# Optimization experiments

Measured on AMD Instinct MI355X. Metric: run time of the kernel, lower is better.

The kernel has to match this reference:

```python
import jax, jax.numpy as jnp
import numpy as np

B, N, Q, H = 32, 1024, 64, 768


def setup_inputs() -> dict:
    key = jax.random.key(0)
    k1, k2, k3, k4 = jax.random.split(key, 4)
    return {
        "nodes_compress": jax.random.normal(k1, (B, N, H), dtype=jnp.float32),
        "query_compress": jax.random.normal(k2, (B, Q, H), dtype=jnp.float32),
        "nodes_hidden": jax.random.normal(k3, (B, N, H), dtype=jnp.float32),
        # nn.Linear(3H, 1, bias=False).weight flattened to (3H,)
        "w": jax.random.normal(k4, (3 * H,), dtype=jnp.float32) * (1.0 / np.sqrt(3 * H)),
    }


def reference(nodes_compress, query_compress, nodes_hidden, w):
    h = nodes_compress.shape[-1]
    w_n, w_q, w_nq = w[:h], w[h:2 * h], w[2 * h:]
    # Decomposed trilinear similarity: identical to Linear([n, q, n*q]) -> scalar
    sim = (
        (nodes_compress @ w_n)[:, :, None]          # (B, N, 1)
        + (query_compress @ w_q)[:, None, :]        # (B, 1, Q)
        + jnp.einsum("bnh,bqh,h->bnq", nodes_compress, query_compress, w_nq)
    )                                                # (B, N, Q)
    # nodes -> query attention
    a = jax.nn.softmax(sim, axis=-1)                 # (B, N, Q)
    nodes2query = jnp.einsum("bnq,bqh->bnh", a, query_compress)
    # query -> nodes attention (max over query, softmax over nodes)
    b = jax.nn.softmax(jnp.max(sim, axis=-1), axis=-1)  # (B, N)
    q2n = jnp.einsum("bn,bnh->bh", b, nodes_compress)[:, None, :]  # (B, 1, H)
    q2n = jnp.broadcast_to(q2n, nodes_compress.shape)               # (B, N, H)
    return jnp.concatenate(
        [nodes_compress, nodes2query, nodes_compress * nodes2query, nodes_compress * q2n],
        axis=-1,
    )  # (B, N, 4H)
```

## Files before the change

kernel.cpp:

```cpp
#include <hip/hip_runtime.h>
#include <hip/hip_bf16.h>

#define BB 32
#define NN 1024
#define QQ 64
#define HH 768

typedef __attribute__((ext_vector_type(8))) short short8;
typedef __attribute__((ext_vector_type(4))) float f32x4;

__device__ __forceinline__ unsigned short f2b(float f) {
  unsigned int u = __float_as_uint(f);
  unsigned int r = u + 0x7fffu + ((u >> 16) & 1u);
  return (unsigned short)(r >> 16);
}

__global__ void k_prep(const float* __restrict__ qc, const float* __restrict__ w,
                       unsigned short* __restrict__ qwB, unsigned short* __restrict__ qcT,
                       float* __restrict__ sq) {
  int bid = blockIdx.x;
  if (bid < 6144) {
    int idx = bid * 256 + threadIdx.x;
    int h = idx % HH;
    qwB[idx] = f2b(qc[idx] * w[2 * HH + h] + w[h]);
    int q2 = idx & 63;
    int h2 = (idx >> 6) % HH;
    int b2 = idx / (HH * QQ);
    qcT[idx] = f2b(qc[(b2 * QQ + q2) * HH + h2]);
  } else {
    int wid = ((bid - 6144) * 256 + threadIdx.x) >> 6;
    int l = threadIdx.x & 63;
    const float* row = qc + (size_t)wid * HH;
    float s = 0.f;
#pragma unroll
    for (int i = 0; i < 12; ++i) s += row[i * 64 + l] * w[HH + i * 64 + l];
#pragma unroll
    for (int m = 1; m < 64; m <<= 1) s += __shfl_xor(s, m);
    if (l == 0) sq[wid] = s;
  }
}

__global__ __launch_bounds__(256) void k_sim(
    const float* __restrict__ nc, const unsigned short* __restrict__ qwB,
    const float* __restrict__ sq, float* __restrict__ partial,
    float* __restrict__ mtse, unsigned short* __restrict__ probs)
{
  __shared__ char smem[32768];
  unsigned short* aLDS = (unsigned short*)smem;
  unsigned short* bLDS = (unsigned short*)(smem + 16384);
  float* rowmF = (float*)(smem + 16384);
  float* wvF   = (float*)(smem + 16384 + 256);

  const int tid = threadIdx.x;
  const int w = tid >> 6, l = tid & 63;
  const int l15 = l & 15, lg = l >> 4;
  const int b = blockIdx.x >> 4, tile = blockIdx.x & 15;
  const int row0 = tile * 64;

  const float* ncB = nc + (size_t)(b * NN + row0) * HH;
  const unsigned short* qwBb = qwB + (size_t)b * QQ * HH;

  f32x4 acc[4] = {};
  for (int kc = 0; kc < 6; ++kc) {
#pragma unroll
    for (int i = 0; i < 4; ++i) {
      int unit = i * 256 + tid;
      int r = unit >> 4, uu = unit & 15;
      const float* src = ncB + r * HH + kc * 128 + uu * 8;
      float4 f0 = *(const float4*)src;
      float4 f1 = *(const float4*)(src + 4);
      short8 v;
      v[0] = (short)f2b(f0.x); v[1] = (short)f2b(f0.y);
      v[2] = (short)f2b(f0.z); v[3] = (short)f2b(f0.w);
      v[4] = (short)f2b(f1.x); v[5] = (short)f2b(f1.y);
      v[6] = (short)f2b(f1.z); v[7] = (short)f2b(f1.w);
      int off = r * 256 + ((uu * 16) ^ ((r & 7) << 4));
      *(short8*)((char*)aLDS + off) = v;
      short8 bv = *(const short8*)(qwBb + r * HH + kc * 128 + uu * 8);
      *(short8*)((char*)bLDS + off) = bv;
    }
    __syncthreads();
#pragma unroll
    for (int ks = 0; ks < 4; ++ks) {
      int kbyte = ks * 64 + lg * 16;
      int arow = w * 16 + l15;
      short8 af = *(short8*)((char*)aLDS + arow * 256 + (kbyte ^ ((l & 7) << 4)));
#pragma unroll
      for (int nt = 0; nt < 4; ++nt) {
        int brow = nt * 16 + l15;
        short8 bf = *(short8*)((char*)bLDS + brow * 256 + (kbyte ^ ((l & 7) << 4)));
        acc[nt] = __builtin_amdgcn_mfma_f32_16x16x32_bf16(af, bf, acc[nt], 0, 0, 0);
      }
      __asm__ volatile("" ::: "memory");
    }
    __syncthreads();
  }

  unsigned short* pT = probs + (size_t)(b * 16 + tile) * (QQ * QQ);
  float sqv[4];
#pragma unroll
  for (int nt = 0; nt < 4; ++nt) sqv[nt] = sq[b * QQ + nt * 16 + l15];
#pragma unroll
  for (int j = 0; j < 4; ++j) {
    float mm = -1e30f;
#pragma unroll
    for (int nt = 0; nt < 4; ++nt) { acc[nt][j] += sqv[nt]; mm = fmaxf(mm, acc[nt][j]); }
    mm = fmaxf(mm, __shfl_xor(mm, 1));
    mm = fmaxf(mm, __shfl_xor(mm, 2));
    mm = fmaxf(mm, __shfl_xor(mm, 4));
    mm = fmaxf(mm, __shfl_xor(mm, 8));
    float ss = 0.f;
#pragma unroll
    for (int nt = 0; nt < 4; ++nt) { float p = __expf(acc[nt][j] - mm); acc[nt][j] = p; ss += p; }
    ss += __shfl_xor(ss, 1); ss += __shfl_xor(ss, 2);
    ss += __shfl_xor(ss, 4); ss += __shfl_xor(ss, 8);
    float inv = 1.0f / ss;
    int r = w * 16 + lg * 4 + j;
#pragma unroll
    for (int nt = 0; nt < 4; ++nt)
      pT[r * 64 + nt * 16 + l15] = f2b(acc[nt][j] * inv);
    if (l15 == 0) rowmF[r] = mm;
  }
  __syncthreads();

  float m_t = -1e30f;
#pragma unroll
  for (int i = 0; i < 16; ++i) {
    f32x4 v = ((f32x4*)rowmF)[i];
    m_t = fmaxf(m_t, fmaxf(fmaxf(v[0], v[1]), fmaxf(v[2], v[3])));
  }
  if (tid < 64) wvF[tid] = __expf(rowmF[tid] - m_t);
  __syncthreads();
  {
    float sv = wvF[l];
#pragma unroll
    for (int m = 1; m < 64; m <<= 1) sv += __shfl_xor(sv, m);
    if (tid == 0) {
      mtse[(b * 16 + tile) * 2] = m_t;
      mtse[(b * 16 + tile) * 2 + 1] = sv;
    }
  }
  {
    float p0 = 0.f, p1 = 0.f, p2 = 0.f;
    for (int n = 0; n < 64; ++n) {
      float wv = wvF[n];
      const float* pr = ncB + n * HH + tid;
      p0 += wv * pr[0]; p1 += wv * pr[256]; p2 += wv * pr[512];
    }
    float* pp = partial + (size_t)(b * 16 + tile) * HH + tid;
    pp[0] = p0; pp[256] = p1; pp[512] = p2;
  }
}

__global__ void k_comb(const float* __restrict__ partial, const float* __restrict__ mtse,
                       float* __restrict__ q2n) {
  int b = blockIdx.x, t = threadIdx.x;
  float mt[16], se[16];
  float M = -1e30f;
#pragma unroll
  for (int i = 0; i < 16; ++i) {
    mt[i] = mtse[(b * 16 + i) * 2];
    se[i] = mtse[(b * 16 + i) * 2 + 1];
    M = fmaxf(M, mt[i]);
  }
  float denom = 0.f;
#pragma unroll
  for (int i = 0; i < 16; ++i) { mt[i] = __expf(mt[i] - M); denom += mt[i] * se[i]; }
  float inv = 1.0f / denom;
  float a0 = 0.f, a1 = 0.f, a2 = 0.f;
#pragma unroll
  for (int i = 0; i < 16; ++i) {
    const float* pp = partial + (size_t)(b * 16 + i) * HH + t;
    float c = mt[i] * inv;
    a0 += c * pp[0]; a1 += c * pp[256]; a2 += c * pp[512];
  }
  q2n[b * HH + t] = a0;
  q2n[b * HH + t + 256] = a1;
  q2n[b * HH + t + 512] = a2;
}

__global__ __launch_bounds__(256) void k_out(
    const float* __restrict__ nc, const unsigned short* __restrict__ qcT,
    const unsigned short* __restrict__ probs, const float* __restrict__ q2n,
    float* __restrict__ out)
{
  __shared__ char smem[16384];

  const int tid = threadIdx.x;
  const int w = tid >> 6, l = tid & 63;
  const int l15 = l & 15, lg = l >> 4;
  const int b = blockIdx.x >> 5;
  const int tile = (blockIdx.x >> 1) & 15;
  const int hh = blockIdx.x & 1;
  const int row0 = tile * 64;

  const unsigned short* pT = probs + (size_t)(b * 16 + tile) * (QQ * QQ);
  short8 a2[2];
  a2[0] = *(const short8*)((const char*)pT + (w * 16 + l15) * 128 + 0 * 64 + lg * 16);
  a2[1] = *(const short8*)((const char*)pT + (w * 16 + l15) * 128 + 1 * 64 + lg * 16);

  const unsigned short* qcTb = qcT + (size_t)b * HH * QQ;
  const int n = w * 16 + l15;
  const float* ncrow = nc + (size_t)(b * NN + row0 + n) * HH;
  float* orow = out + (size_t)(b * NN + row0 + n) * 3072;
  const float* q2nb = q2n + b * HH;

  for (int hc = hh * 3; hc < hh * 3 + 3; ++hc) {
#pragma unroll
    for (int i = 0; i < 4; ++i) {
      int unit = i * 256 + tid;
      int r = unit >> 3, uu = unit & 7;
      short8 v = *(const short8*)(qcTb + (size_t)(hc * 128 + r) * 64 + uu * 8);
      int off = r * 128 + ((uu * 16) ^ ((r & 7) << 4));
      *(short8*)(smem + off) = v;
    }
    __syncthreads();
#pragma unroll
    for (int hg = 0; hg < 8; ++hg) {
      f32x4 c2 = {};
#pragma unroll
      for (int ks2 = 0; ks2 < 2; ++ks2) {
        int hrow = hg * 16 + l15;
        int kbyte = ks2 * 64 + lg * 16;
        short8 hf = *(short8*)(smem + hrow * 128 + (kbyte ^ ((l & 7) << 4)));
        c2 = __builtin_amdgcn_mfma_f32_16x16x32_bf16(hf, a2[ks2], c2, 0, 0, 0);
      }
      int hbase = hc * 128 + hg * 16 + lg * 4;
      f32x4 ncv = *(const f32x4*)(ncrow + hbase);
      f32x4 qv  = *(const f32x4*)(q2nb + hbase);
      __builtin_nontemporal_store(ncv,       (f32x4*)(orow + hbase));
      __builtin_nontemporal_store(c2,        (f32x4*)(orow + HH + hbase));
      __builtin_nontemporal_store(ncv * c2,  (f32x4*)(orow + 2 * HH + hbase));
      __builtin_nontemporal_store(ncv * qv,  (f32x4*)(orow + 2304 + hbase));
    }
    __syncthreads();
  }
}

extern "C" void kernel_launch(void* const* d_in, const int* in_sizes, int n_in,
                              void* d_out, int out_size, void* d_ws, size_t ws_size,
                              hipStream_t stream) {
  (void)in_sizes; (void)n_in; (void)out_size; (void)ws_size;
  const float* nc = (const float*)d_in[0];
  const float* qc = (const float*)d_in[1];
  const float* w  = (const float*)d_in[3];
  float* out = (float*)d_out;
  char* ws = (char*)d_ws;
  unsigned short* qwB = (unsigned short*)(ws);
  unsigned short* qcT = (unsigned short*)(ws + 3145728);
  float* sqv     = (float*)(ws + 6291456);
  float* partial = (float*)(ws + 6299648);
  float* mtse    = (float*)(ws + 7872512);
  float* q2n     = (float*)(ws + 7876608);
  unsigned short* probs = (unsigned short*)(ws + 7975424);

  k_prep<<<6656, 256, 0, stream>>>(qc, w, qwB, qcT, sqv);
  k_sim<<<512, 256, 0, stream>>>(nc, qwB, sqv, partial, mtse, probs);
  k_comb<<<32, 256, 0, stream>>>(partial, mtse, q2n);
  k_out<<<1024, 256, 0, stream>>>(nc, qcT, probs, q2n, out);
}
```

Baseline: 188.8 us.

## Fuse query weighting into sim kernel, split output kernel finer, drop nontemporal stores

```diff
diff --git a/kernel.cpp b/kernel.cpp
--- a/kernel.cpp
+++ b/kernel.cpp
@@ -16,13 +16,10 @@
 }
 
 __global__ void k_prep(const float* __restrict__ qc, const float* __restrict__ w,
-                       unsigned short* __restrict__ qwB, unsigned short* __restrict__ qcT,
-                       float* __restrict__ sq) {
+                       unsigned short* __restrict__ qcT, float* __restrict__ sq) {
   int bid = blockIdx.x;
   if (bid < 6144) {
     int idx = bid * 256 + threadIdx.x;
-    int h = idx % HH;
-    qwB[idx] = f2b(qc[idx] * w[2 * HH + h] + w[h]);
     int q2 = idx & 63;
     int h2 = (idx >> 6) % HH;
     int b2 = idx / (HH * QQ);
@@ -41,9 +38,10 @@
 }
 
 __global__ __launch_bounds__(256) void k_sim(
-    const float* __restrict__ nc, const unsigned short* __restrict__ qwB,
-    const float* __restrict__ sq, float* __restrict__ partial,
-    float* __restrict__ mtse, unsigned short* __restrict__ probs)
+    const float* __restrict__ nc, const float* __restrict__ qc,
+    const float* __restrict__ w, const float* __restrict__ sq,
+    float* __restrict__ partial, float* __restrict__ mtse,
+    unsigned short* __restrict__ probs)
 {
   __shared__ char smem[32768];
   unsigned short* aLDS = (unsigned short*)smem;
@@ -52,13 +50,13 @@
   float* wvF   = (float*)(smem + 16384 + 256);
 
   const int tid = threadIdx.x;
-  const int w = tid >> 6, l = tid & 63;
+  const int wv_ = tid >> 6, l = tid & 63;
   const int l15 = l & 15, lg = l >> 4;
   const int b = blockIdx.x >> 4, tile = blockIdx.x & 15;
   const int row0 = tile * 64;
 
   const float* ncB = nc + (size_t)(b * NN + row0) * HH;
-  const unsigned short* qwBb = qwB + (size_t)b * QQ * HH;
+  const float* qcB = qc + (size_t)b * QQ * HH;
 
   f32x4 acc[4] = {};
   for (int kc = 0; kc < 6; ++kc) {
@@ -66,7 +64,8 @@
     for (int i = 0; i < 4; ++i) {
       int unit = i * 256 + tid;
       int r = unit >> 4, uu = unit & 15;
-      const float* src = ncB + r * HH + kc * 128 + uu * 8;
+      int h = kc * 128 + uu * 8;
+      const float* src = ncB + r * HH + h;
       float4 f0 = *(const float4*)src;
       float4 f1 = *(const float4*)(src + 4);
       short8 v;
@@ -76,14 +75,25 @@
       v[6] = (short)f2b(f1.z); v[7] = (short)f2b(f1.w);
       int off = r * 256 + ((uu * 16) ^ ((r & 7) << 4));
       *(short8*)((char*)aLDS + off) = v;
-      short8 bv = *(const short8*)(qwBb + r * HH + kc * 128 + uu * 8);
+      const float* qsrc = qcB + r * HH + h;
+      float4 g0 = *(const float4*)qsrc;
+      float4 g1 = *(const float4*)(qsrc + 4);
+      float4 wn0 = *(const float4*)(w + h);
+      float4 wn1 = *(const float4*)(w + h + 4);
+      float4 wm0 = *(const float4*)(w + 2 * HH + h);
+      float4 wm1 = *(const float4*)(w + 2 * HH + h + 4);
+      short8 bv;
+      bv[0] = (short)f2b(g0.x * wm0.x + wn0.x); bv[1] = (short)f2b(g0.y * wm0.y + wn0.y);
+      bv[2] = (short)f2b(g0.z * wm0.z + wn0.z); bv[3] = (short)f2b(g0.w * wm0.w + wn0.w);
+      bv[4] = (short)f2b(g1.x * wm1.x + wn1.x); bv[5] = (short)f2b(g1.y * wm1.y + wn1.y);
+      bv[6] = (short)f2b(g1.z * wm1.z + wn1.z); bv[7] = (short)f2b(g1.w * wm1.w + wn1.w);
       *(short8*)((char*)bLDS + off) = bv;
     }
     __syncthreads();
 #pragma unroll
     for (int ks = 0; ks < 4; ++ks) {
       int kbyte = ks * 64 + lg * 16;
-      int arow = w * 16 + l15;
+      int arow = wv_ * 16 + l15;
       short8 af = *(short8*)((char*)aLDS + arow * 256 + (kbyte ^ ((l & 7) << 4)));
 #pragma unroll
       for (int nt = 0; nt < 4; ++nt) {
@@ -115,7 +125,7 @@
     ss += __shfl_xor(ss, 1); ss += __shfl_xor(ss, 2);
     ss += __shfl_xor(ss, 4); ss += __shfl_xor(ss, 8);
     float inv = 1.0f / ss;
-    int r = w * 16 + lg * 4 + j;
+    int r = wv_ * 16 + lg * 4 + j;
 #pragma unroll
     for (int nt = 0; nt < 4; ++nt)
       pT[r * 64 + nt * 16 + l15] = f2b(acc[nt][j] * inv);
@@ -143,9 +153,9 @@
   {
     float p0 = 0.f, p1 = 0.f, p2 = 0.f;
     for (int n = 0; n < 64; ++n) {
-      float wv = wvF[n];
+      float wvv = wvF[n];
       const float* pr = ncB + n * HH + tid;
-      p0 += wv * pr[0]; p1 += wv * pr[256]; p2 += wv * pr[512];
+      p0 += wvv * pr[0]; p1 += wvv * pr[256]; p2 += wvv * pr[512];
     }
     float* pp = partial + (size_t)(b * 16 + tile) * HH + tid;
     pp[0] = p0; pp[256] = p1; pp[512] = p2;
@@ -187,53 +197,51 @@
   __shared__ char smem[16384];
 
   const int tid = threadIdx.x;
-  const int w = tid >> 6, l = tid & 63;
+  const int wv_ = tid >> 6, l = tid & 63;
   const int l15 = l & 15, lg = l >> 4;
-  const int b = blockIdx.x >> 5;
-  const int tile = (blockIdx.x >> 1) & 15;
-  const int hh = blockIdx.x & 1;
+  const int bid = blockIdx.x;
+  const int hc = bid % 6;
+  const int bt = bid / 6;
+  const int b = bt >> 4, tile = bt & 15;
   const int row0 = tile * 64;
 
-  const unsigned short* pT = probs + (size_t)(b * 16 + tile) * (QQ * QQ);
+  const unsigned short* pT = probs + (size_t)bt * (QQ * QQ);
   short8 a2[2];
-  a2[0] = *(const short8*)((const char*)pT + (w * 16 + l15) * 128 + 0 * 64 + lg * 16);
-  a2[1] = *(const short8*)((const char*)pT + (w * 16 + l15) * 128 + 1 * 64 + lg * 16);
+  a2[0] = *(const short8*)((const char*)pT + (wv_ * 16 + l15) * 128 + 0 * 64 + lg * 16);
+  a2[1] = *(const short8*)((const char*)pT + (wv_ * 16 + l15) * 128 + 1 * 64 + lg * 16);
 
   const unsigned short* qcTb = qcT + (size_t)b * HH * QQ;
-  const int n = w * 16 + l15;
+  const int n = wv_ * 16 + l15;
   const float* ncrow = nc + (size_t)(b * NN + row0 + n) * HH;
   float* orow = out + (size_t)(b * NN + row0 + n) * 3072;
   const float* q2nb = q2n + b * HH;
 
-  for (int hc = hh * 3; hc < hh * 3 + 3; ++hc) {
-#pragma unroll
-    for (int i = 0; i < 4; ++i) {
-      int unit = i * 256 + tid;
-      int r = unit >> 3, uu = unit & 7;
-      short8 v = *(const short8*)(qcTb + (size_t)(hc * 128 + r) * 64 + uu * 8);
-      int off = r * 128 + ((uu * 16) ^ ((r & 7) << 4));
-      *(short8*)(smem + off) = v;
-    }
-    __syncthreads();
-#pragma unroll
-    for (int hg = 0; hg < 8; ++hg) {
-      f32x4 c2 = {};
-#pragma unroll
-      for (int ks2 = 0; ks2 < 2; ++ks2) {
-        int hrow = hg * 16 + l15;
-        int kbyte = ks2 * 64 + lg * 16;
-        short8 hf = *(short8*)(smem + hrow * 128 + (kbyte ^ ((l & 7) << 4)));
-        c2 = __builtin_amdgcn_mfma_f32_16x16x32_bf16(hf, a2[ks2], c2, 0, 0, 0);
-      }
-      int hbase = hc * 128 + hg * 16 + lg * 4;
-      f32x4 ncv = *(const f32x4*)(ncrow + hbase);
-      f32x4 qv  = *(const f32x4*)(q2nb + hbase);
-      __builtin_nontemporal_store(ncv,       (f32x4*)(orow + hbase));
-      __builtin_nontemporal_store(c2,        (f32x4*)(orow + HH + hbase));
-      __builtin_nontemporal_store(ncv * c2,  (f32x4*)(orow + 2 * HH + hbase));
-      __builtin_nontemporal_store(ncv * qv,  (f32x4*)(orow + 2304 + hbase));
-    }
-    __syncthreads();
+#pragma unroll
+  for (int i = 0; i < 4; ++i) {
+    int unit = i * 256 + tid;
+    int r = unit >> 3, uu = unit & 7;
+    short8 v = *(const short8*)(qcTb + (size_t)(hc * 128 + r) * 64 + uu * 8);
+    int off = r * 128 + ((uu * 16) ^ ((r & 7) << 4));
+    *(short8*)(smem + off) = v;
+  }
+  __syncthreads();
+#pragma unroll
+  for (int hg = 0; hg < 8; ++hg) {
+    f32x4 c2 = {};
+#pragma unroll
+    for (int ks2 = 0; ks2 < 2; ++ks2) {
+      int hrow = hg * 16 + l15;
+      int kbyte = ks2 * 64 + lg * 16;
+      short8 hf = *(short8*)(smem + hrow * 128 + (kbyte ^ ((l & 7) << 4)));
+      c2 = __builtin_amdgcn_mfma_f32_16x16x32_bf16(hf, a2[ks2], c2, 0, 0, 0);
+    }
+    int hbase = hc * 128 + hg * 16 + lg * 4;
+    f32x4 ncv = *(const f32x4*)(ncrow + hbase);
+    f32x4 qv  = *(const f32x4*)(q2nb + hbase);
+    *(f32x4*)(orow + hbase)            = ncv;
+    *(f32x4*)(orow + HH + hbase)       = c2;
+    *(f32x4*)(orow + 2 * HH + hbase)   = ncv * c2;
+    *(f32x4*)(orow + 2304 + hbase)     = ncv * qv;
   }
 }
 
@@ -246,16 +254,15 @@
   const float* w  = (const float*)d_in[3];
   float* out = (float*)d_out;
   char* ws = (char*)d_ws;
-  unsigned short* qwB = (unsigned short*)(ws);
-  unsigned short* qcT = (unsigned short*)(ws + 3145728);
-  float* sqv     = (float*)(ws + 6291456);
-  float* partial = (float*)(ws + 6299648);
-  float* mtse    = (float*)(ws + 7872512);
-  float* q2n     = (float*)(ws + 7876608);
-  unsigned short* probs = (unsigned short*)(ws + 7975424);
-
-  k_prep<<<6656, 256, 0, stream>>>(qc, w, qwB, qcT, sqv);
-  k_sim<<<512, 256, 0, stream>>>(nc, qwB, sqv, partial, mtse, probs);
+  unsigned short* qcT = (unsigned short*)(ws);
+  float* sqv     = (float*)(ws + 3145728);
+  float* partial = (float*)(ws + 3153920);
+  float* mtse    = (float*)(ws + 4726784);
+  float* q2n     = (float*)(ws + 4730880);
+  unsigned short* probs = (unsigned short*)(ws + 4829184);
+
+  k_prep<<<6656, 256, 0, stream>>>(qc, w, qcT, sqv);
+  k_sim<<<512, 256, 0, stream>>>(nc, qc, w, sqv, partial, mtse, probs);
   k_comb<<<32, 256, 0, stream>>>(partial, mtse, q2n);
-  k_out<<<1024, 256, 0, stream>>>(nc, qcT, probs, q2n, out);
-}
+  k_out<<<3072, 256, 0, stream>>>(nc, qcT, probs, q2n, out);
+}
```

After: 179.4 us. 5.0% less time.
